# Performance work log

Measured on AMD Instinct MI355X. Metric: run time of the kernel, lower is better.

## Reference

```python
import jax, jax.numpy as jnp
import numpy as np
from jax import lax


def _conv2d(x, w, pad=1):
    # x: (N,C,H,W), w: (O,I,kh,kw) -> (N,O,H,W)
    return lax.conv_general_dilated(
        x, w, window_strides=(1, 1), padding=[(pad, pad), (pad, pad)],
        dimension_numbers=("NCHW", "OIHW", "NCHW"))


def setup_inputs() -> dict:
    key = jax.random.key(0)
    ks = jax.random.split(key, 5)
    B, T, C, H, W = 4, 8, 256, 64, 64
    DH = 128
    fan = C * 3 * 3
    x = jax.random.normal(ks[0], (B, T, C, H, W), dtype=jnp.float32)
    w_k = jax.random.normal(ks[1], (DH, C, 3, 3), dtype=jnp.float32) * (2.0 / fan) ** 0.5
    w_q = jax.random.normal(ks[2], (DH, C, 3, 3), dtype=jnp.float32) * (2.0 / fan) ** 0.5
    w_v = jax.random.normal(ks[3], (DH, C, 3, 3), dtype=jnp.float32) * (2.0 / fan) ** 0.5
    w_out = jax.random.normal(ks[4], (C, DH, 3, 3), dtype=jnp.float32) * (2.0 / (DH * 9)) ** 0.5
    b_out = jnp.zeros((C,), dtype=jnp.float32)
    return {"x": x, "w_k": w_k, "w_q": w_q, "w_v": w_v, "w_out": w_out, "b_out": b_out}


def reference(x, w_k, w_q, w_v, w_out, b_out):
    B, T, C, H, W = x.shape
    DH = w_k.shape[0]
    # key comes only from the first frame
    k = _conv2d(x[:, 0], w_k)                                  # (B,DH,H,W)
    xf = x.reshape(B * T, C, H, W)
    q = _conv2d(xf, w_q).reshape(B, T, DH, H, W)               # (B,T,DH,H,W)
    v = _conv2d(xf, w_v).reshape(B, T, DH, H, W)
    # per-pixel channel dot between each frame's q and the single k
    dots = jnp.einsum("btchw,bchw->bthw", q, k)                # (B,T,H,W)
    attn = jax.nn.softmax(dots, axis=1)                        # softmax over T
    pooled = jnp.einsum("bthw,btchw->bchw", attn, v)           # (B,DH,H,W)
    # out conv applied once (result is identical for every repeated frame)
    out = _conv2d(pooled, w_out) + b_out[None, :, None, None]  # (B,C,H,W)
    return jnp.broadcast_to(out[:, None], (B, T, C, H, W))
```

## Files before the change

### kernel.cpp

```cpp
#include <hip/hip_runtime.h>
#include <cstdint>
#include <cstddef>

#define NB 4
#define NT 8
#define NC 256
#define NDH 128
#define HWs 4096

typedef _Float16 f16;
typedef _Float16 f16x8 __attribute__((ext_vector_type(8)));
typedef float f32x16 __attribute__((ext_vector_type(16)));


__device__ __forceinline__ void gload16(const void* g, void* l) {
    __builtin_amdgcn_global_load_lds(
        (const __attribute__((address_space(1))) void*)g,
        (__attribute__((address_space(3))) void*)l, 16, 0, 0);
}

__global__ __launch_bounds__(256) void prep_x_kernel(const float* __restrict__ x,
                                                     f16* __restrict__ xh) {
    __shared__ f16 sxt[256 * 66];
    int bt = blockIdx.x >> 6, h = blockIdx.x & 63;
    int tid = threadIdx.x;
    int w = tid & 63, c4 = tid >> 6;
    for (int p = 0; p < 64; ++p) {
        int c = p * 4 + c4;
        sxt[c * 66 + w] = (f16)x[(((size_t)bt * NC + c) * 64 + h) * 64 + w];
    }
    __syncthreads();
    int cg = tid & 31, wb = tid >> 5;
    f16x8* xh8 = (f16x8*)xh;
    for (int p = 0; p < 8; ++p) {
        int w2 = wb * 8 + p;
        f16x8 v;
        #pragma unroll
        for (int j = 0; j < 8; ++j) v[j] = sxt[(cg * 8 + j) * 66 + w2];
        xh8[((size_t)(bt * 64 + h) * 64 + w2) * 32 + cg] = v;
    }
}

__global__ __launch_bounds__(256) void prep_w_kernel(const float* __restrict__ w,
                                                     f16* __restrict__ wt2,
                                                     int OC, int CIN) {
    int CG = CIN >> 3;
    int idx = blockIdx.x * 256 + threadIdx.x;
    if (idx >= OC * CG) return;
    int oc = idx / CG, cg = idx - oc * CG;
    f16x8* wt8 = (f16x8*)wt2;
    #pragma unroll
    for (int tap = 0; tap < 9; ++tap) {
        f16x8 v;
        #pragma unroll
        for (int j = 0; j < 8; ++j)
            v[j] = (f16)w[((size_t)oc * CIN + cg * 8 + j) * 9 + tap];
        wt8[((size_t)tap * CG + cg) * OC + oc] = v;
    }
}

template <int CIN>
__device__ __forceinline__ void conv_core2(const f16x8* __restrict__ xh8,
                                           const f16x8* __restrict__ wt8,
                                           int OCT, int oc0, int h0,
                                           f16x8* __restrict__ sxb,
                                           f16x8* __restrict__ swb,
                                           f32x16 acc[2][2][2]) {
    const int tid = threadIdx.x;
    const int lane = tid & 63;
    const int wv = tid >> 6;
    const int n = lane & 31, q = lane >> 5;
    const int CG = CIN / 8;
    const int NI = CIN / 16;

    #pragma unroll
    for (int oi = 0; oi < 2; ++oi)
        #pragma unroll
        for (int rr = 0; rr < 2; ++rr)
            #pragma unroll
            for (int ct = 0; ct < 2; ++ct)
                #pragma unroll
                for (int r = 0; r < 16; ++r) acc[oi][rr][ct][r] = 0.0f;

    f16x8 Z8 = {(f16)0, (f16)0, (f16)0, (f16)0, (f16)0, (f16)0, (f16)0, (f16)0};

    #pragma unroll
    for (int bufi = 0; bufi < 2; ++bufi) {
        f16x8* sx8 = sxb + bufi * 1320;
        if (tid < 40) {
            int r = tid >> 2, k = tid & 3;
            sx8[r * 132 + (k >> 1) * 130 + (k & 1)] = Z8;
        }
        for (int r = 0; r < 10; ++r) {
            int h = h0 - 1 + r;
            if ((unsigned)h >= 64u && tid < 132) sx8[r * 132 + tid] = Z8;
        }
    }

    auto stage = [&](f16x8* sx8, f16x8* sw8, int cg0) {
        for (int j = wv; j < 18; j += 4) {
            int tap = j >> 1, qh = j & 1;
            gload16(wt8 + (size_t)(tap * CG + cg0 + qh) * OCT + oc0 + lane,
                    sw8 + (tap * 2 + qh) * 64);
        }
        for (int j = wv; j < 20; j += 4) {
            int r = j >> 1, cb = j & 1;
            int h = h0 - 1 + r;
            if ((unsigned)h < 64u) {
                int col = cb * 32 + (lane >> 1);
                int cidx = col + 1;
                int cg = cg0 + ((lane & 1) ^ ((cidx >> 2) & 1));
                gload16(xh8 + (size_t)(h * 64 + col) * CG + cg,
                        sx8 + r * 132 + 2 + cb * 64);
            }
        }
    };

    stage(sxb, swb, 0);
    asm volatile("s_waitcnt vmcnt(0)" ::: "memory");
    __syncthreads();

    for (int it = 0; it < NI; ++it) {
        f16x8* sx8 = sxb + (it & 1) * 1320;
        f16x8* sw8 = swb + (it & 1) * 1152;
        if (it + 1 < NI)
            stage(sxb + ((it + 1) & 1) * 1320, swb + ((it + 1) & 1) * 1152,
                  (it + 1) * 2);
        #pragma unroll
        for (int tap = 0; tap < 9; ++tap) {
            const int ky = tap / 3, kx = tap % 3;
            f16x8 a0 = sw8[(tap * 2 + q) * 64 + n];
            f16x8 a1 = sw8[(tap * 2 + q) * 64 + 32 + n];
            #pragma unroll
            for (int rr = 0; rr < 2; ++rr) {
                const int r = wv * 2 + rr + ky;
                #pragma unroll
                for (int ct = 0; ct < 2; ++ct) {
                    int cidx = ct * 32 + n + kx;
                    int s = q ^ ((cidx >> 2) & 1);
                    f16x8 b = sx8[r * 132 + cidx * 2 + s];
                    acc[0][rr][ct] = __builtin_amdgcn_mfma_f32_32x32x16_f16(a0, b, acc[0][rr][ct], 0, 0, 0);
                    acc[1][rr][ct] = __builtin_amdgcn_mfma_f32_32x32x16_f16(a1, b, acc[1][rr][ct], 0, 0, 0);
                }
            }
        }
        asm volatile("s_waitcnt vmcnt(0)" ::: "memory");
        __syncthreads();
    }
}

__global__ __launch_bounds__(256, 2) void conv_k_kernel(const f16* __restrict__ xh,
        const f16* __restrict__ wk2, float* __restrict__ kbuf) {
    __shared__ f16x8 sxb[2640];
    __shared__ f16x8 swb[2304];
    int bx = blockIdx.x;
    int b = bx >> 4, ocg = (bx >> 3) & 1, hb = bx & 7;
    int h0 = hb * 8, oc0 = ocg * 64;
    int bt = b * NT;
    f32x16 acc[2][2][2];
    conv_core2<NC>((const f16x8*)xh + (size_t)bt * 64 * 64 * 32, (const f16x8*)wk2,
                   NDH, oc0, h0, sxb, swb, acc);
    int lane = threadIdx.x & 63, wv = threadIdx.x >> 6;
    int n = lane & 31, q = lane >> 5;
    #pragma unroll
    for (int rr = 0; rr < 2; ++rr) {
        int h = h0 + wv * 2 + rr;
        #pragma unroll
        for (int oi = 0; oi < 2; ++oi)
            #pragma unroll
            for (int r = 0; r < 16; ++r) {
                int oc = oc0 + oi * 32 + 4 * q + (r & 3) + 8 * (r >> 2);
                float* kp = kbuf + ((size_t)(b * NDH + oc)) * HWs + h * 64;
                kp[n] = acc[oi][rr][0][r];
                kp[32 + n] = acc[oi][rr][1][r];
            }
    }
}

__global__ __launch_bounds__(256, 2) void conv_q_kernel(const f16* __restrict__ xh,
        const f16* __restrict__ wq2, const float* __restrict__ kbuf,
        float* __restrict__ qpart) {
    __shared__ f16x8 sxb[2640];
    __shared__ f16x8 swb[2304];
    int bx = blockIdx.x;
    int bt = bx >> 4, ocg = (bx >> 3) & 1, hb = bx & 7;
    int b = bt >> 3;
    int h0 = hb * 8, oc0 = ocg * 64;
    f32x16 acc[2][2][2];
    conv_core2<NC>((const f16x8*)xh + (size_t)bt * 64 * 64 * 32, (const f16x8*)wq2,
                   NDH, oc0, h0, sxb, swb, acc);
    int lane = threadIdx.x & 63, wv = threadIdx.x >> 6;
    int n = lane & 31, q = lane >> 5;
    #pragma unroll
    for (int rr = 0; rr < 2; ++rr) {
        int h = h0 + wv * 2 + rr;
        float p0 = 0.0f, p1 = 0.0f;
        #pragma unroll
        for (int oi = 0; oi < 2; ++oi)
            #pragma unroll
            for (int r = 0; r < 16; ++r) {
                int oc = oc0 + oi * 32 + 4 * q + (r & 3) + 8 * (r >> 2);
                const float* kp = kbuf + ((size_t)(b * NDH + oc)) * HWs + h * 64;
                p0 += acc[oi][rr][0][r] * kp[n];
                p1 += acc[oi][rr][1][r] * kp[32 + n];
            }
        p0 += __shfl_xor(p0, 32, 64);
        p1 += __shfl_xor(p1, 32, 64);
        if (q == 0) {
            qpart[((size_t)ocg * 32 + bt) * HWs + h * 64 + n] = p0;
            qpart[((size_t)ocg * 32 + bt) * HWs + h * 64 + 32 + n] = p1;
        }
    }
}

__global__ __launch_bounds__(256) void softmax_t_kernel(const float* __restrict__ qpart,
                                                        float* __restrict__ dots) {
    int idx = blockIdx.x * 256 + threadIdx.x;
    int b = idx >> 12;
    int p = idx & 4095;
    const float* q0 = qpart + (size_t)(b * NT) * HWs + p;
    const float* q1 = qpart + (size_t)(32 + b * NT) * HWs + p;
    float v[NT];
    float m = -3.4e38f;
    #pragma unroll
    for (int t = 0; t < NT; ++t) { v[t] = q0[t * HWs] + q1[t * HWs]; m = fmaxf(m, v[t]); }
    float s = 0.0f;
    #pragma unroll
    for (int t = 0; t < NT; ++t) { v[t] = __expf(v[t] - m); s += v[t]; }
    float inv = 1.0f / s;
    float* base = dots + (size_t)b * NT * HWs + p;
    #pragma unroll
    for (int t = 0; t < NT; ++t) base[t * HWs] = v[t] * inv;
}

__global__ __launch_bounds__(256, 2) void conv_v_kernel(const f16* __restrict__ xh,
        const f16* __restrict__ wv2, const float* __restrict__ attn,
        f16* __restrict__ parts) {
    __shared__ f16x8 sxb[2640];
    __shared__ f16x8 swb[2304];
    int bx = blockIdx.x;
    int bt = bx >> 4, ocg = (bx >> 3) & 1, hb = bx & 7;
    int b = bt >> 3, t = bt & 7;
    int h0 = hb * 8, oc0 = ocg * 64;
    f32x16 acc[2][2][2];
    conv_core2<NC>((const f16x8*)xh + (size_t)bt * 64 * 64 * 32, (const f16x8*)wv2,
                   NDH, oc0, h0, sxb, swb, acc);
    int lane = threadIdx.x & 63, wv = threadIdx.x >> 6;
    int n = lane & 31, q = lane >> 5;
    f16* pp = parts + (size_t)(t * NB + b) * NDH * HWs;
    #pragma unroll
    for (int rr = 0; rr < 2; ++rr) {
        int h = h0 + wv * 2 + rr;
        float a0 = attn[(size_t)bt * HWs + h * 64 + n];
        float a1 = attn[(size_t)bt * HWs + h * 64 + 32 + n];
        #pragma unroll
        for (int oi = 0; oi < 2; ++oi)
            #pragma unroll
            for (int r = 0; r < 16; ++r) {
                int oc = oc0 + oi * 32 + 4 * q + (r & 3) + 8 * (r >> 2);
                f16* op = pp + (size_t)oc * HWs + h * 64;
                op[n] = (f16)(a0 * acc[oi][rr][0][r]);
                op[32 + n] = (f16)(a1 * acc[oi][rr][1][r]);
            }
    }
}

__global__ __launch_bounds__(256) void prep_pooled_kernel(const f16* __restrict__ parts,
                                                          f16* __restrict__ pooledT) {
    __shared__ f16 sxt[128 * 66];
    int b = blockIdx.x >> 6, h = blockIdx.x & 63;
    int tid = threadIdx.x, w = tid & 63, c4 = tid >> 6;
    for (int p = 0; p < 32; ++p) {
        int c = p * 4 + c4;
        float s = 0.0f;
        #pragma unroll
        for (int t = 0; t < NT; ++t)
            s += (float)parts[(((size_t)(t * NB + b) * NDH + c)) * HWs + h * 64 + w];
        sxt[c * 66 + w] = (f16)s;
    }
    __syncthreads();
    int cg = tid & 15, wb = tid >> 4;
    f16x8* pt8 = (f16x8*)pooledT;
    for (int p = 0; p < 4; ++p) {
        int w2 = wb * 4 + p;
        f16x8 v;
        #pragma unroll
        for (int j = 0; j < 8; ++j) v[j] = sxt[(cg * 8 + j) * 66 + w2];
        pt8[((size_t)(b * 64 + h) * 64 + w2) * 16 + cg] = v;
    }
}

__global__ __launch_bounds__(256, 2) void conv_out_kernel(const f16* __restrict__ pooledT,
        const f16* __restrict__ wo2, const float* __restrict__ b_out,
        float* __restrict__ out) {
    __shared__ f16x8 sxb[2640];
    __shared__ f16x8 swb[2304];
    int bx = blockIdx.x;
    int b = bx >> 5, ocg = (bx >> 3) & 3, hb = bx & 7;
    int h0 = hb * 8, oc0 = ocg * 64;
    f32x16 acc[2][2][2];
    conv_core2<NDH>((const f16x8*)pooledT + (size_t)b * 64 * 64 * 16, (const f16x8*)wo2,
                    NC, oc0, h0, sxb, swb, acc);
    int lane = threadIdx.x & 63, wv = threadIdx.x >> 6;
    int n = lane & 31, q = lane >> 5;
    #pragma unroll
    for (int rr = 0; rr < 2; ++rr) {
        int h = h0 + wv * 2 + rr;
        #pragma unroll
        for (int oi = 0; oi < 2; ++oi)
            #pragma unroll
            for (int r = 0; r < 16; ++r) {
                int oc = oc0 + oi * 32 + 4 * q + (r & 3) + 8 * (r >> 2);
                float bias = b_out[oc];
                float v0 = acc[oi][rr][0][r] + bias;
                float v1 = acc[oi][rr][1][r] + bias;
                for (int t = 0; t < NT; ++t) {
                    float* op = out + ((size_t)(b * NT + t) * NC + oc) * HWs + h * 64;
                    op[n] = v0;
                    op[32 + n] = v1;
                }
            }
    }
}

extern "C" void kernel_launch(void* const* d_in, const int* in_sizes, int n_in,
                              void* d_out, int out_size, void* d_ws, size_t ws_size,
                              hipStream_t stream) {
    (void)in_sizes; (void)n_in; (void)out_size; (void)ws_size;
    const float* x     = (const float*)d_in[0];
    const float* w_k   = (const float*)d_in[1];
    const float* w_q   = (const float*)d_in[2];
    const float* w_v   = (const float*)d_in[3];
    const float* w_out = (const float*)d_in[4];
    const float* b_out = (const float*)d_in[5];
    float* out = (float*)d_out;

    char* ws = (char*)d_ws;
    f16*   xh      = (f16*)ws;
    float* kbuf    = (float*)(ws + 67108864);
    float* dots    = (float*)(ws + 75497472);
    f16*   parts   = (f16*)(ws + 76021760);
    float* qpart   = (float*)(ws + 76021760);
    f16*   pooledT = (f16*)(ws + 109576192);
    f16*   wq2     = (f16*)(ws + 113770496);
    f16*   wk2     = (f16*)(ws + 114360320);
    f16*   wv2     = (f16*)(ws + 114950144);
    f16*   wo2     = (f16*)(ws + 115539968);

    hipLaunchKernelGGL(prep_x_kernel, dim3(2048), dim3(256), 0, stream, x, xh);
    hipLaunchKernelGGL(prep_w_kernel, dim3(16), dim3(256), 0, stream, w_q, wq2, NDH, NC);
    hipLaunchKernelGGL(prep_w_kernel, dim3(16), dim3(256), 0, stream, w_k, wk2, NDH, NC);
    hipLaunchKernelGGL(prep_w_kernel, dim3(16), dim3(256), 0, stream, w_v, wv2, NDH, NC);
    hipLaunchKernelGGL(prep_w_kernel, dim3(16), dim3(256), 0, stream, w_out, wo2, NC, NDH);

    hipLaunchKernelGGL(conv_k_kernel, dim3(NB * 2 * 8), dim3(256), 0, stream, xh, wk2, kbuf);
    hipLaunchKernelGGL(conv_q_kernel, dim3(NB * NT * 2 * 8), dim3(256), 0, stream, xh, wq2, kbuf, qpart);
    hipLaunchKernelGGL(softmax_t_kernel, dim3(64), dim3(256), 0, stream, qpart, dots);
    hipLaunchKernelGGL(conv_v_kernel, dim3(NB * NT * 2 * 8), dim3(256), 0, stream, xh, wv2, dots, parts);
    hipLaunchKernelGGL(prep_pooled_kernel, dim3(256), dim3(256), 0, stream, parts, pooledT);
    hipLaunchKernelGGL(conv_out_kernel, dim3(NB * 4 * 8), dim3(256), 0, stream, pooledT, wo2, b_out, out);
}
```

Measured before the change: 501.7 us.

## Merge output-channel groups into 512-thread blocks sharing staged input tiles

Each conv block now runs 8 waves covering both (or two) 64-channel groups, so the staged input row tile in LDS is shared across twice as many output channels instead of being loaded by separate blocks. Weight staging doubles per block, grids halve, and block IDs are remapped with an XCD-aware swizzle. MFMA sections are wrapped in s_setprio, and the explicit vmcnt waits are dropped. The trade is fewer blocks (only 32 for conv_k and 64 for conv_out), which lowers parallelism across CUs. Removing the explicit vmcnt waits before the barriers also risks reading LDS before the async global-to-LDS loads have landed.

```diff
diff --git a/kernel.cpp b/kernel.cpp
--- a/kernel.cpp
+++ b/kernel.cpp
@@ -17,6 +17,11 @@
     __builtin_amdgcn_global_load_lds(
         (const __attribute__((address_space(1))) void*)g,
         (__attribute__((address_space(3))) void*)l, 16, 0, 0);
+}
+
+__device__ __forceinline__ int xcd_swz(int bid, int nwg) {
+    int q = nwg >> 3;
+    return (bid & 7) * q + (bid >> 3);
 }
 
 __global__ __launch_bounds__(256) void prep_x_kernel(const float* __restrict__ x,
@@ -60,7 +65,7 @@
 }
 
 template <int CIN>
-__device__ __forceinline__ void conv_core2(const f16x8* __restrict__ xh8,
+__device__ __forceinline__ void conv_core3(const f16x8* __restrict__ xh8,
                                            const f16x8* __restrict__ wt8,
                                            int OCT, int oc0, int h0,
                                            f16x8* __restrict__ sxb,
@@ -69,6 +74,7 @@
     const int tid = threadIdx.x;
     const int lane = tid & 63;
     const int wv = tid >> 6;
+    const int ocg = wv >> 2, rp = wv & 3;
     const int n = lane & 31, q = lane >> 5;
     const int CG = CIN / 8;
     const int NI = CIN / 16;
@@ -84,26 +90,27 @@
 
     f16x8 Z8 = {(f16)0, (f16)0, (f16)0, (f16)0, (f16)0, (f16)0, (f16)0, (f16)0};
 
-    #pragma unroll
-    for (int bufi = 0; bufi < 2; ++bufi) {
-        f16x8* sx8 = sxb + bufi * 1320;
-        if (tid < 40) {
-            int r = tid >> 2, k = tid & 3;
-            sx8[r * 132 + (k >> 1) * 130 + (k & 1)] = Z8;
+    if (tid < 80) {
+        int buf = tid / 40, rem = tid - buf * 40;
+        int r = rem >> 2, k = rem & 3;
+        sxb[buf * 1320 + r * 132 + (k >> 1) * 130 + (k & 1)] = Z8;
+    }
+    if (h0 == 0 && tid < 264) {
+        int buf = tid / 132, c = tid - buf * 132;
+        sxb[buf * 1320 + c] = Z8;
+    }
+    if (h0 == 56 && tid < 264) {
+        int buf = tid / 132, c = tid - buf * 132;
+        sxb[buf * 1320 + 9 * 132 + c] = Z8;
+    }
+
+    auto stage = [&](f16x8* sx8, f16x8* sw8, int cg0) {
+        for (int j = wv; j < 36; j += 8) {
+            int tap = j >> 2, qh = (j >> 1) & 1, hf = j & 1;
+            gload16(wt8 + (size_t)(tap * CG + cg0 + qh) * OCT + oc0 + hf * 64 + lane,
+                    sw8 + (tap * 2 + qh) * 128 + hf * 64);
         }
-        for (int r = 0; r < 10; ++r) {
-            int h = h0 - 1 + r;
-            if ((unsigned)h >= 64u && tid < 132) sx8[r * 132 + tid] = Z8;
-        }
-    }
-
-    auto stage = [&](f16x8* sx8, f16x8* sw8, int cg0) {
-        for (int j = wv; j < 18; j += 4) {
-            int tap = j >> 1, qh = j & 1;
-            gload16(wt8 + (size_t)(tap * CG + cg0 + qh) * OCT + oc0 + lane,
-                    sw8 + (tap * 2 + qh) * 64);
-        }
-        for (int j = wv; j < 20; j += 4) {
+        for (int j = wv; j < 20; j += 8) {
             int r = j >> 1, cb = j & 1;
             int h = h0 - 1 + r;
             if ((unsigned)h < 64u) {
@@ -117,23 +124,24 @@
     };
 
     stage(sxb, swb, 0);
-    asm volatile("s_waitcnt vmcnt(0)" ::: "memory");
     __syncthreads();
 
     for (int it = 0; it < NI; ++it) {
         f16x8* sx8 = sxb + (it & 1) * 1320;
-        f16x8* sw8 = swb + (it & 1) * 1152;
+        f16x8* sw8 = swb + (it & 1) * 2304;
         if (it + 1 < NI)
-            stage(sxb + ((it + 1) & 1) * 1320, swb + ((it + 1) & 1) * 1152,
+            stage(sxb + ((it + 1) & 1) * 1320, swb + ((it + 1) & 1) * 2304,
                   (it + 1) * 2);
+
+        __builtin_amdgcn_s_setprio(1);
         #pragma unroll
         for (int tap = 0; tap < 9; ++tap) {
             const int ky = tap / 3, kx = tap % 3;
-            f16x8 a0 = sw8[(tap * 2 + q) * 64 + n];
-            f16x8 a1 = sw8[(tap * 2 + q) * 64 + 32 + n];
+            f16x8 a0 = sw8[(tap * 2 + q) * 128 + ocg * 64 + n];
+            f16x8 a1 = sw8[(tap * 2 + q) * 128 + ocg * 64 + 32 + n];
             #pragma unroll
             for (int rr = 0; rr < 2; ++rr) {
-                const int r = wv * 2 + rr + ky;
+                const int r = rp * 2 + rr + ky;
                 #pragma unroll
                 for (int ct = 0; ct < 2; ++ct) {
                     int cidx = ct * 32 + n + kx;
@@ -144,32 +152,33 @@
                 }
             }
         }
-        asm volatile("s_waitcnt vmcnt(0)" ::: "memory");
+        __builtin_amdgcn_s_setprio(0);
         __syncthreads();
     }
 }
 
-__global__ __launch_bounds__(256, 2) void conv_k_kernel(const f16* __restrict__ xh,
+__global__ __launch_bounds__(512, 2) void conv_k_kernel(const f16* __restrict__ xh,
         const f16* __restrict__ wk2, float* __restrict__ kbuf) {
-    __shared__ f16x8 sxb[2640];
-    __shared__ f16x8 swb[2304];
-    int bx = blockIdx.x;
-    int b = bx >> 4, ocg = (bx >> 3) & 1, hb = bx & 7;
-    int h0 = hb * 8, oc0 = ocg * 64;
+    __shared__ f16x8 sxb[2 * 1320];
+    __shared__ f16x8 swb[2 * 2304];
+    int s = xcd_swz(blockIdx.x, NB * 8);
+    int b = s >> 3, hb = s & 7;
+    int h0 = hb * 8;
     int bt = b * NT;
     f32x16 acc[2][2][2];
-    conv_core2<NC>((const f16x8*)xh + (size_t)bt * 64 * 64 * 32, (const f16x8*)wk2,
-                   NDH, oc0, h0, sxb, swb, acc);
+    conv_core3<NC>((const f16x8*)xh + (size_t)bt * 64 * 64 * 32, (const f16x8*)wk2,
+                   NDH, 0, h0, sxb, swb, acc);
     int lane = threadIdx.x & 63, wv = threadIdx.x >> 6;
+    int ocg = wv >> 2, rp = wv & 3;
     int n = lane & 31, q = lane >> 5;
     #pragma unroll
     for (int rr = 0; rr < 2; ++rr) {
-        int h = h0 + wv * 2 + rr;
+        int h = h0 + rp * 2 + rr;
         #pragma unroll
         for (int oi = 0; oi < 2; ++oi)
             #pragma unroll
             for (int r = 0; r < 16; ++r) {
-                int oc = oc0 + oi * 32 + 4 * q + (r & 3) + 8 * (r >> 2);
+                int oc = ocg * 64 + oi * 32 + 4 * q + (r & 3) + 8 * (r >> 2);
                 float* kp = kbuf + ((size_t)(b * NDH + oc)) * HWs + h * 64;
                 kp[n] = acc[oi][rr][0][r];
                 kp[32 + n] = acc[oi][rr][1][r];
@@ -177,29 +186,30 @@
     }
 }
 
-__global__ __launch_bounds__(256, 2) void conv_q_kernel(const f16* __restrict__ xh,
+__global__ __launch_bounds__(512, 2) void conv_q_kernel(const f16* __restrict__ xh,
         const f16* __restrict__ wq2, const float* __restrict__ kbuf,
         float* __restrict__ qpart) {
-    __shared__ f16x8 sxb[2640];
-    __shared__ f16x8 swb[2304];
-    int bx = blockIdx.x;
-    int bt = bx >> 4, ocg = (bx >> 3) & 1, hb = bx & 7;
+    __shared__ f16x8 sxb[2 * 1320];
+    __shared__ f16x8 swb[2 * 2304];
+    int s = xcd_swz(blockIdx.x, NB * NT * 8);
+    int bt = s >> 3, hb = s & 7;
     int b = bt >> 3;
-    int h0 = hb * 8, oc0 = ocg * 64;
+    int h0 = hb * 8;
     f32x16 acc[2][2][2];
-    conv_core2<NC>((const f16x8*)xh + (size_t)bt * 64 * 64 * 32, (const f16x8*)wq2,
-                   NDH, oc0, h0, sxb, swb, acc);
+    conv_core3<NC>((const f16x8*)xh + (size_t)bt * 64 * 64 * 32, (const f16x8*)wq2,
+                   NDH, 0, h0, sxb, swb, acc);
     int lane = threadIdx.x & 63, wv = threadIdx.x >> 6;
+    int ocg = wv >> 2, rp = wv & 3;
     int n = lane & 31, q = lane >> 5;
     #pragma unroll
     for (int rr = 0; rr < 2; ++rr) {
-        int h = h0 + wv * 2 + rr;
+        int h = h0 + rp * 2 + rr;
         float p0 = 0.0f, p1 = 0.0f;
         #pragma unroll
         for (int oi = 0; oi < 2; ++oi)
             #pragma unroll
             for (int r = 0; r < 16; ++r) {
-                int oc = oc0 + oi * 32 + 4 * q + (r & 3) + 8 * (r >> 2);
+                int oc = ocg * 64 + oi * 32 + 4 * q + (r & 3) + 8 * (r >> 2);
                 const float* kp = kbuf + ((size_t)(b * NDH + oc)) * HWs + h * 64;
                 p0 += acc[oi][rr][0][r] * kp[n];
                 p1 += acc[oi][rr][1][r] * kp[32 + n];
@@ -233,31 +243,32 @@
     for (int t = 0; t < NT; ++t) base[t * HWs] = v[t] * inv;
 }
 
-__global__ __launch_bounds__(256, 2) void conv_v_kernel(const f16* __restrict__ xh,
+__global__ __launch_bounds__(512, 2) void conv_v_kernel(const f16* __restrict__ xh,
         const f16* __restrict__ wv2, const float* __restrict__ attn,
         f16* __restrict__ parts) {
-    __shared__ f16x8 sxb[2640];
-    __shared__ f16x8 swb[2304];
-    int bx = blockIdx.x;
-    int bt = bx >> 4, ocg = (bx >> 3) & 1, hb = bx & 7;
+    __shared__ f16x8 sxb[2 * 1320];
+    __shared__ f16x8 swb[2 * 2304];
+    int s = xcd_swz(blockIdx.x, NB * NT * 8);
+    int bt = s >> 3, hb = s & 7;
     int b = bt >> 3, t = bt & 7;
-    int h0 = hb * 8, oc0 = ocg * 64;
+    int h0 = hb * 8;
     f32x16 acc[2][2][2];
-    conv_core2<NC>((const f16x8*)xh + (size_t)bt * 64 * 64 * 32, (const f16x8*)wv2,
-                   NDH, oc0, h0, sxb, swb, acc);
+    conv_core3<NC>((const f16x8*)xh + (size_t)bt * 64 * 64 * 32, (const f16x8*)wv2,
+                   NDH, 0, h0, sxb, swb, acc);
     int lane = threadIdx.x & 63, wv = threadIdx.x >> 6;
+    int ocg = wv >> 2, rp = wv & 3;
     int n = lane & 31, q = lane >> 5;
     f16* pp = parts + (size_t)(t * NB + b) * NDH * HWs;
     #pragma unroll
     for (int rr = 0; rr < 2; ++rr) {
-        int h = h0 + wv * 2 + rr;
+        int h = h0 + rp * 2 + rr;
         float a0 = attn[(size_t)bt * HWs + h * 64 + n];
         float a1 = attn[(size_t)bt * HWs + h * 64 + 32 + n];
         #pragma unroll
         for (int oi = 0; oi < 2; ++oi)
             #pragma unroll
             for (int r = 0; r < 16; ++r) {
-                int oc = oc0 + oi * 32 + 4 * q + (r & 3) + 8 * (r >> 2);
+                int oc = ocg * 64 + oi * 32 + 4 * q + (r & 3) + 8 * (r >> 2);
                 f16* op = pp + (size_t)oc * HWs + h * 64;
                 op[n] = (f16)(a0 * acc[oi][rr][0][r]);
                 op[32 + n] = (f16)(a1 * acc[oi][rr][1][r]);
@@ -290,27 +301,28 @@
     }
 }
 
-__global__ __launch_bounds__(256, 2) void conv_out_kernel(const f16* __restrict__ pooledT,
+__global__ __launch_bounds__(512, 2) void conv_out_kernel(const f16* __restrict__ pooledT,
         const f16* __restrict__ wo2, const float* __restrict__ b_out,
         float* __restrict__ out) {
-    __shared__ f16x8 sxb[2640];
-    __shared__ f16x8 swb[2304];
-    int bx = blockIdx.x;
-    int b = bx >> 5, ocg = (bx >> 3) & 3, hb = bx & 7;
-    int h0 = hb * 8, oc0 = ocg * 64;
+    __shared__ f16x8 sxb[2 * 1320];
+    __shared__ f16x8 swb[2 * 2304];
+    int s = xcd_swz(blockIdx.x, NB * 2 * 8);
+    int b = s >> 4, oh = (s >> 3) & 1, hb = s & 7;
+    int h0 = hb * 8, oc0 = oh * 128;
     f32x16 acc[2][2][2];
-    conv_core2<NDH>((const f16x8*)pooledT + (size_t)b * 64 * 64 * 16, (const f16x8*)wo2,
+    conv_core3<NDH>((const f16x8*)pooledT + (size_t)b * 64 * 64 * 16, (const f16x8*)wo2,
                     NC, oc0, h0, sxb, swb, acc);
     int lane = threadIdx.x & 63, wv = threadIdx.x >> 6;
+    int ocg = wv >> 2, rp = wv & 3;
     int n = lane & 31, q = lane >> 5;
     #pragma unroll
     for (int rr = 0; rr < 2; ++rr) {
-        int h = h0 + wv * 2 + rr;
+        int h = h0 + rp * 2 + rr;
         #pragma unroll
         for (int oi = 0; oi < 2; ++oi)
             #pragma unroll
             for (int r = 0; r < 16; ++r) {
-                int oc = oc0 + oi * 32 + 4 * q + (r & 3) + 8 * (r >> 2);
+                int oc = oc0 + ocg * 64 + oi * 32 + 4 * q + (r & 3) + 8 * (r >> 2);
                 float bias = b_out[oc];
                 float v0 = acc[oi][rr][0][r] + bias;
                 float v1 = acc[oi][rr][1][r] + bias;
@@ -353,10 +365,10 @@
     hipLaunchKernelGGL(prep_w_kernel, dim3(16), dim3(256), 0, stream, w_v, wv2, NDH, NC);
     hipLaunchKernelGGL(prep_w_kernel, dim3(16), dim3(256), 0, stream, w_out, wo2, NC, NDH);
 
-    hipLaunchKernelGGL(conv_k_kernel, dim3(NB * 2 * 8), dim3(256), 0, stream, xh, wk2, kbuf);
-    hipLaunchKernelGGL(conv_q_kernel, dim3(NB * NT * 2 * 8), dim3(256), 0, stream, xh, wq2, kbuf, qpart);
+    hipLaunchKernelGGL(conv_k_kernel, dim3(NB * 8), dim3(512), 0, stream, xh, wk2, kbuf);
+    hipLaunchKernelGGL(conv_q_kernel, dim3(NB * NT * 8), dim3(512), 0, stream, xh, wq2, kbuf, qpart);
     hipLaunchKernelGGL(softmax_t_kernel, dim3(64), dim3(256), 0, stream, qpart, dots);
-    hipLaunchKernelGGL(conv_v_kernel, dim3(NB * NT * 2 * 8), dim3(256), 0, stream, xh, wv2, dots, parts);
+    hipLaunchKernelGGL(conv_v_kernel, dim3(NB * NT * 8), dim3(512), 0, stream, xh, wv2, dots, parts);
     hipLaunchKernelGGL(prep_pooled_kernel, dim3(256), dim3(256), 0, stream, parts, pooledT);
-    hipLaunchKernelGGL(conv_out_kernel, dim3(NB * 4 * 8), dim3(256), 0, stream, pooledT, wo2, b_out, out);
-}
+    hipLaunchKernelGGL(conv_out_kernel, dim3(NB * 2 * 8), dim3(512), 0, stream, pooledT, wo2, b_out, out);
+}
```

Result: slower. 533.8 us (+6.4%).
